# Kernel optimization log

Hardware: AMD Instinct MI355X
Metric: run time of the kernel (lower is better)

Reference implementation:

```python
import jax, jax.numpy as jnp
import numpy as np

R, B, F, H, C = 32, 2048, 512, 1024, 100  # n_rules, batch, n_fea, 2*n_fea, n_cls


def setup_inputs() -> dict:
    key = jax.random.key(0)
    ks = jax.random.split(key, 10)
    sc = lambda k, shape, fan: (jax.random.normal(k, shape, jnp.float32) / np.float32(np.sqrt(fan)))
    return {
        "data": jax.random.normal(ks[0], (B, F), jnp.float32),
        "proto": jax.random.normal(ks[1], (R, F), jnp.float32),
        "var": jax.random.uniform(ks[2], (R, F), jnp.float32, 0.5, 1.5),
        "fs_w1": sc(ks[3], (F, H), F), "fs_b1": jnp.zeros((H,), jnp.float32),
        "fs_w2": sc(ks[4], (H, F), H), "fs_b2": jnp.zeros((F,), jnp.float32),
        "fs_w3": sc(ks[5], (F, 1), F), "fs_b3": jnp.zeros((1,), jnp.float32),
        "cq_w1": sc(ks[6], (R, F, H), F), "cq_b1": jnp.zeros((R, H), jnp.float32),
        "cq_w2": sc(ks[7], (R, H, F), H), "cq_b2": jnp.zeros((R, F), jnp.float32),
        "cq_w3": sc(ks[8], (R, F, C), F), "cq_b3": jnp.zeros((R, C), jnp.float32),
        "is_train": 1,
    }


def reference(data, proto, var, fs_w1, fs_b1, fs_w2, fs_b2, fs_w3, fs_b3,
              cq_w1, cq_b1, cq_w2, cq_b2, cq_w3, cq_b3, is_train):
    # Gaussian fuzzy membership per rule: [R, B, F]
    fuzzy = jnp.exp(-(data[None, :, :] - proto[:, None, :]) ** 2
                    / (2.0 * var[:, None, :] ** 2))
    # shared fire-strength MLP applied per rule
    h = jax.nn.relu(jnp.einsum('rbf,fh->rbh', fuzzy, fs_w1) + fs_b1)
    h = jax.nn.relu(jnp.einsum('rbh,hf->rbf', h, fs_w2) + fs_b2)
    fs_logits = (jnp.einsum('rbf,fo->rbo', h, fs_w3) + fs_b3)[..., 0]  # [R, B]
    fire = jax.nn.softmax(fs_logits.T, axis=1)  # [B, R], softmax over rules
    # per-rule consequent MLPs on raw data (grouped GEMMs)
    g = jax.nn.relu(jnp.einsum('bf,rfh->rbh', data, cq_w1) + cq_b1[:, None, :])
    g = jax.nn.relu(jnp.einsum('rbh,rhf->rbf', g, cq_w2) + cq_b2[:, None, :])
    logits = jnp.einsum('rbf,rfc->rbc', g, cq_w3) + cq_b3[:, None, :]  # [R, B, C]
    # softmax-weighted expert sum, then class softmax
    out = jnp.einsum('br,rbc->bc', fire, logits)  # [B, C]
    return jax.nn.softmax(out, axis=1)
```

## Files before the change

kernel.cpp:

```cpp
#include <hip/hip_runtime.h>

typedef __attribute__((ext_vector_type(8))) short short8;
typedef __attribute__((ext_vector_type(4))) float f32x4;

__device__ __forceinline__ unsigned short f2bf(float f) {
    union { float f; unsigned u; } v; v.f = f;
    unsigned r = v.u + 0x7FFFu + ((v.u >> 16) & 1u);
    return (unsigned short)(r >> 16);
}
__device__ __forceinline__ float bf2f(unsigned short u) {
    union { unsigned u; float f; } v; v.u = ((unsigned)u) << 16;
    return v.f;
}

__global__ __launch_bounds__(256)
void cvt_bf16_kernel(const float* __restrict__ X, unsigned short* __restrict__ Y, int n4) {
    int i = blockIdx.x * 256 + threadIdx.x;
    if (i >= n4) return;
    float4 v = ((const float4*)X)[i];
    ushort4 o; o.x = f2bf(v.x); o.y = f2bf(v.y); o.z = f2bf(v.z); o.w = f2bf(v.w);
    ((ushort4*)Y)[i] = o;
}

__global__ __launch_bounds__(256)
void transpose_kernel(const float* __restrict__ X, unsigned short* __restrict__ Y,
                      int K, int N, int Np) {
    __shared__ float tile[32][33];
    int g = blockIdx.z;
    const float* Xg = X + (long)g * K * N;
    unsigned short* Yg = Y + (long)g * Np * K;
    int k0 = blockIdx.x * 32, n0 = blockIdx.y * 32;
    int tx = threadIdx.x & 31, ty = threadIdx.x >> 5;
#pragma unroll
    for (int i = 0; i < 4; ++i) {
        int kk = ty + i * 8;
        int n = n0 + tx;
        tile[kk][tx] = (n < N) ? Xg[(long)(k0 + kk) * N + n] : 0.0f;
    }
    __syncthreads();
#pragma unroll
    for (int i = 0; i < 4; ++i) {
        int nn = ty + i * 8;
        Yg[(long)(n0 + nn) * K + k0 + tx] = f2bf(tile[tx][nn]);
    }
}

__global__ __launch_bounds__(128)
void fuzzy_kernel(const float* __restrict__ data, const float* __restrict__ proto,
                  const float* __restrict__ var, unsigned short* __restrict__ fuzzy,
                  int r0) {
    int rb = blockIdx.x;
    int r = r0 + (rb >> 11), b = rb & 2047;
    int f = threadIdx.x * 4;
    float4 d = *(const float4*)(data + (long)b * 512 + f);
    float4 p = *(const float4*)(proto + (long)r * 512 + f);
    float4 w = *(const float4*)(var + (long)r * 512 + f);
    ushort4 o;
    float x;
    x = d.x - p.x; o.x = f2bf(__expf(-(x * x) / (2.f * w.x * w.x)));
    x = d.y - p.y; o.y = f2bf(__expf(-(x * x) / (2.f * w.y * w.y)));
    x = d.z - p.z; o.z = f2bf(__expf(-(x * x) / (2.f * w.z * w.z)));
    x = d.w - p.w; o.w = f2bf(__expf(-(x * x) / (2.f * w.w * w.w)));
    *(ushort4*)(fuzzy + (long)rb * 512 + f) = o;
}

template<int EPI, bool RELU>
__global__ __launch_bounds__(256, 2)
void gemm_kernel(const unsigned short* __restrict__ A,
                 const unsigned short* __restrict__ Bt,
                 const float* __restrict__ bias,
                 void* __restrict__ Cptr,
                 const float* __restrict__ w3,
                 float* __restrict__ fslog,
                 int nM, int nN, int K,
                 long sAg, long sBg, long sCg, int sBiasG, int biasN) {
    unsigned tot = gridDim.x;
    unsigned bid = blockIdx.x;
    unsigned sw = (tot & 7u) == 0 ? (bid & 7u) * (tot >> 3) + (bid >> 3) : bid;
    unsigned pg = (unsigned)nM * (unsigned)nN;
    unsigned g = sw / pg;
    unsigned rem = sw - g * pg;
    unsigned mt_ = rem / (unsigned)nN;
    unsigned nt_ = rem - mt_ * (unsigned)nN;
    const int N = nN * 128;
    A += (long)g * sAg;
    Bt += (long)g * sBg;
    bias += (long)g * sBiasG;
    const int m0 = (int)mt_ * 128;
    const int n0 = (int)nt_ * 128;

    __shared__ __align__(16) unsigned short ldsA[128 * 32];
    __shared__ __align__(16) unsigned short ldsB[128 * 32];

    const int tid = threadIdx.x;
    const int lane = tid & 63;
    const int w = tid >> 6;
    const int wm = w >> 1, wn = w & 1;
    const int r16 = lane & 15, kg = lane >> 4;

    f32x4 acc[4][4];
#pragma unroll
    for (int i = 0; i < 4; ++i)
#pragma unroll
        for (int j = 0; j < 4; ++j) {
            f32x4 z = {0.f, 0.f, 0.f, 0.f};
            acc[i][j] = z;
        }

    for (int k0 = 0; k0 < K; k0 += 32) {
#pragma unroll
        for (int j = 0; j < 2; ++j) {
            int t = j * 256 + tid;
            int row = t >> 2, kc = (t & 3) * 8;
            const unsigned short* ga = A + (long)(m0 + row) * K + k0 + kc;
            __builtin_amdgcn_global_load_lds(
                (const __attribute__((address_space(1))) void*)ga,
                (__attribute__((address_space(3))) void*)(ldsA + (j * 256 + w * 64) * 8),
                16, 0, 0);
            const unsigned short* gb = Bt + (long)(n0 + row) * K + k0 + kc;
            __builtin_amdgcn_global_load_lds(
                (const __attribute__((address_space(1))) void*)gb,
                (__attribute__((address_space(3))) void*)(ldsB + (j * 256 + w * 64) * 8),
                16, 0, 0);
        }
        __syncthreads();
        short8 aF[4], bF[4];
#pragma unroll
        for (int mt = 0; mt < 4; ++mt)
            aF[mt] = *(const short8*)(ldsA + (wm * 64 + mt * 16 + r16) * 32 + kg * 8);
#pragma unroll
        for (int nt = 0; nt < 4; ++nt)
            bF[nt] = *(const short8*)(ldsB + (wn * 64 + nt * 16 + r16) * 32 + kg * 8);
#pragma unroll
        for (int mt = 0; mt < 4; ++mt)
#pragma unroll
            for (int nt = 0; nt < 4; ++nt)
                acc[mt][nt] = __builtin_amdgcn_mfma_f32_16x16x32_bf16(
                    aF[mt], bF[nt], acc[mt][nt], 0, 0, 0);
        __syncthreads();
    }

    if constexpr (EPI == 1) {
        float w3v[4], bv[4];
#pragma unroll
        for (int nt = 0; nt < 4; ++nt) {
            int col = n0 + wn * 64 + nt * 16 + r16;
            w3v[nt] = w3[col];
            bv[nt] = bias[col];
        }
#pragma unroll
        for (int mt = 0; mt < 4; ++mt) {
#pragma unroll
            for (int j = 0; j < 4; ++j) {
                float p = 0.f;
#pragma unroll
                for (int nt = 0; nt < 4; ++nt) {
                    float v = acc[mt][nt][j] + bv[nt];
                    if (RELU) v = fmaxf(v, 0.f);
                    p += v * w3v[nt];
                }
                p += __shfl_xor(p, 1, 64);
                p += __shfl_xor(p, 2, 64);
                p += __shfl_xor(p, 4, 64);
                p += __shfl_xor(p, 8, 64);
                if (r16 == 0) {
                    int row = m0 + wm * 64 + mt * 16 + kg * 4 + j;
                    atomicAdd(&fslog[row], p);
                }
            }
        }
    } else {
#pragma unroll
        for (int nt = 0; nt < 4; ++nt) {
            int col = n0 + wn * 64 + nt * 16 + r16;
            float bv = (col < biasN) ? bias[col] : 0.f;
#pragma unroll
            for (int mt = 0; mt < 4; ++mt) {
#pragma unroll
                for (int j = 0; j < 4; ++j) {
                    int row = m0 + wm * 64 + mt * 16 + kg * 4 + j;
                    float v = acc[mt][nt][j] + bv;
                    if (RELU) v = fmaxf(v, 0.f);
                    if constexpr (EPI == 0)
                        ((unsigned short*)Cptr)[(long)g * sCg + (long)row * N + col] = f2bf(v);
                    else
                        ((float*)Cptr)[(long)g * sCg + (long)row * N + col] = v;
                }
            }
        }
    }
}

__global__ __launch_bounds__(256)
void fire_kernel(const float* __restrict__ fslog, float* __restrict__ fire) {
    int b = blockIdx.x * 256 + threadIdx.x;
    float v[32];
    float mx = -1e30f;
#pragma unroll
    for (int r = 0; r < 32; ++r) { v[r] = fslog[r * 2048 + b]; mx = fmaxf(mx, v[r]); }
    float s = 0.f;
#pragma unroll
    for (int r = 0; r < 32; ++r) { v[r] = __expf(v[r] - mx); s += v[r]; }
    float inv = 1.f / s;
#pragma unroll
    for (int r = 0; r < 32; ++r) fire[b * 32 + r] = v[r] * inv;
}

__global__ __launch_bounds__(128)
void accum_kernel(const float* __restrict__ logits, const float* __restrict__ fire,
                  float* __restrict__ mix, int r0, int NR, int first) {
    int b = blockIdx.x, c = threadIdx.x;
    float acc = first ? 0.f : mix[b * 128 + c];
    for (int r = 0; r < NR; ++r)
        acc += fire[b * 32 + r0 + r] * logits[((long)r * 2048 + b) * 128 + c];
    mix[b * 128 + c] = acc;
}

__global__ __launch_bounds__(128)
void softmax_out_kernel(const float* __restrict__ mix, float* __restrict__ out) {
    int b = blockIdx.x, c = threadIdx.x;
    __shared__ float redm[2], reds[2];
    float val = (c < 100) ? mix[b * 128 + c] : -1e30f;
    float m = val;
#pragma unroll
    for (int off = 32; off; off >>= 1) m = fmaxf(m, __shfl_xor(m, off, 64));
    int lane = c & 63, wv = c >> 6;
    if (lane == 0) redm[wv] = m;
    __syncthreads();
    m = fmaxf(redm[0], redm[1]);
    float e = (c < 100) ? __expf(val - m) : 0.f;
    float s = e;
#pragma unroll
    for (int off = 32; off; off >>= 1) s += __shfl_xor(s, off, 64);
    if (lane == 0) reds[wv] = s;
    __syncthreads();
    s = reds[0] + reds[1];
    if (c < 100) out[b * 100 + c] = e / s;
}

extern "C" void kernel_launch(void* const* d_in, const int* in_sizes, int n_in,
                              void* d_out, int out_size, void* d_ws, size_t ws_size,
                              hipStream_t stream) {
    const float* data  = (const float*)d_in[0];
    const float* proto = (const float*)d_in[1];
    const float* var   = (const float*)d_in[2];
    const float* fs_w1 = (const float*)d_in[3];
    const float* fs_b1 = (const float*)d_in[4];
    const float* fs_w2 = (const float*)d_in[5];
    const float* fs_b2 = (const float*)d_in[6];
    const float* fs_w3 = (const float*)d_in[7];
    const float* cq_w1 = (const float*)d_in[9];
    const float* cq_b1 = (const float*)d_in[10];
    const float* cq_w2 = (const float*)d_in[11];
    const float* cq_b2 = (const float*)d_in[12];
    const float* cq_w3 = (const float*)d_in[13];
    const float* cq_b3 = (const float*)d_in[14];
    float* out = (float*)d_out;

    const size_t PERSIST = 2097152 + 1048576 + 1048576 + 262144 + 262144 + 1048576;
    const size_t PER_RULE_P2 = 1048576 + 1048576 + 131072 + 2097152;
    auto need = [&](int p1r, int p2r) -> size_t {
        size_t logitsC = (size_t)p2r * 2048 * 128 * 4;
        size_t R0 = (size_t)p1r * 2048 * 512 * 2;
        size_t r0p2 = (size_t)p2r * PER_RULE_P2;
        if (r0p2 > R0) R0 = r0p2;
        size_t R1 = (size_t)p1r * 2048 * 1024 * 2;
        size_t g1b = (size_t)p2r * 2048 * 1024 * 2;
        if (g1b > R1) R1 = g1b;
        return PERSIST + logitsC + R0 + R1;
    };
    int p1r = 32, p2r = 16;
    while (need(p1r, p2r) > ws_size && p1r > 2) { p1r >>= 1; p2r >>= 1; }

    char* ws = (char*)d_ws;
    size_t off = 0;
    auto take = [&](size_t bytes) { char* p = ws + off; off += bytes; return p; };
    unsigned short* data_bf = (unsigned short*)take(2097152);
    unsigned short* w1t     = (unsigned short*)take(1048576);
    unsigned short* w2t     = (unsigned short*)take(1048576);
    float*          fslog   = (float*)take(262144);
    float*          fire    = (float*)take(262144);
    float*          mix     = (float*)take(1048576);
    float*          logitsC = (float*)take((size_t)p2r * 2048 * 128 * 4);
    size_t R0sz = (size_t)p1r * 2048 * 512 * 2;
    { size_t t = (size_t)p2r * PER_RULE_P2; if (t > R0sz) R0sz = t; }
    char* R0 = take(R0sz);
    size_t R1sz = (size_t)p1r * 2048 * 1024 * 2;
    char* R1 = take(R1sz);

    unsigned short* cF   = (unsigned short*)R0;
    unsigned short* cW1t = (unsigned short*)R0;
    unsigned short* cW2t = (unsigned short*)(R0 + (size_t)p2r * 1048576);
    unsigned short* cW3t = (unsigned short*)(R0 + (size_t)p2r * 2097152);
    unsigned short* g2   = (unsigned short*)(R0 + (size_t)p2r * 2097152 + (size_t)p2r * 131072);
    unsigned short* h1   = (unsigned short*)R1;
    unsigned short* g1   = (unsigned short*)R1;

    cvt_bf16_kernel<<<1024, 256, 0, stream>>>(data, data_bf, 262144);
    transpose_kernel<<<dim3(16, 32, 1), 256, 0, stream>>>(fs_w1, w1t, 512, 1024, 1024);
    transpose_kernel<<<dim3(32, 16, 1), 256, 0, stream>>>(fs_w2, w2t, 1024, 512, 512);
    hipMemsetAsync(fslog, 0, 262144, stream);

    for (int ch = 0; ch < 32 / p1r; ++ch) {
        const int r0 = ch * p1r;
        fuzzy_kernel<<<p1r * 2048, 128, 0, stream>>>(data, proto, var, cF, r0);
        gemm_kernel<0, true><<<p1r * 16 * 8, 256, 0, stream>>>(
            cF, w1t, fs_b1, h1, nullptr, nullptr,
            p1r * 16, 8, 512, 0, 0, 0, 0, 1024);
        gemm_kernel<1, true><<<p1r * 16 * 4, 256, 0, stream>>>(
            h1, w2t, fs_b2, nullptr, fs_w3, fslog + (long)r0 * 2048,
            p1r * 16, 4, 1024, 0, 0, 0, 0, 512);
    }
    fire_kernel<<<8, 256, 0, stream>>>(fslog, fire);

    for (int ch = 0; ch < 32 / p2r; ++ch) {
        const int r0 = ch * p2r;
        transpose_kernel<<<dim3(16, 32, p2r), 256, 0, stream>>>(
            cq_w1 + (long)r0 * 512 * 1024, cW1t, 512, 1024, 1024);
        transpose_kernel<<<dim3(32, 16, p2r), 256, 0, stream>>>(
            cq_w2 + (long)r0 * 1024 * 512, cW2t, 1024, 512, 512);
        transpose_kernel<<<dim3(16, 4, p2r), 256, 0, stream>>>(
            cq_w3 + (long)r0 * 512 * 100, cW3t, 512, 100, 128);
        gemm_kernel<0, true><<<16 * 8 * p2r, 256, 0, stream>>>(
            data_bf, cW1t, cq_b1 + (long)r0 * 1024, g1, nullptr, nullptr,
            16, 8, 512, 0, (long)1024 * 512, (long)2048 * 1024, 1024, 1024);
        gemm_kernel<0, true><<<16 * 4 * p2r, 256, 0, stream>>>(
            g1, cW2t, cq_b2 + (long)r0 * 512, g2, nullptr, nullptr,
            16, 4, 1024, (long)2048 * 1024, (long)512 * 1024, (long)2048 * 512, 512, 512);
        gemm_kernel<2, false><<<16 * 1 * p2r, 256, 0, stream>>>(
            g2, cW3t, cq_b3 + (long)r0 * 100, logitsC, nullptr, nullptr,
            16, 1, 512, (long)2048 * 512, (long)128 * 512, (long)2048 * 128, 100, 100);
        accum_kernel<<<2048, 128, 0, stream>>>(logitsC, fire, mix, r0, p2r, ch == 0);
    }
    softmax_out_kernel<<<2048, 128, 0, stream>>>(mix, out);
}
```

Measured before the change: 549.8 us.

## Swizzle LDS tiles, stage GEMM output via LDS, fuse fire-weighted accumulation into GEMM

GEMM tiles in LDS now use an XOR swizzle on the k-chunk index, meant to cut bank conflicts on fragment reads. The bf16 epilogue is staged through a padded LDS tile so global stores become coalesced 16-byte writes. The separate accumulation kernel is removed: the final consequent GEMM atomically adds fire-weighted logits into the mix buffer, so the logitsC buffer is no longer written. The fire-strength path now processes all 32 rules in a single launch instead of chunks. These changes cost extra LDS per block and add many float atomics, and the atomic accumulation order is no longer fixed.

```diff
diff --git a/kernel.cpp b/kernel.cpp
--- a/kernel.cpp
+++ b/kernel.cpp
@@ -7,10 +7,6 @@
     union { float f; unsigned u; } v; v.f = f;
     unsigned r = v.u + 0x7FFFu + ((v.u >> 16) & 1u);
     return (unsigned short)(r >> 16);
-}
-__device__ __forceinline__ float bf2f(unsigned short u) {
-    union { unsigned u; float f; } v; v.u = ((unsigned)u) << 16;
-    return v.f;
 }
 
 __global__ __launch_bounds__(256)
@@ -47,10 +43,9 @@
 
 __global__ __launch_bounds__(128)
 void fuzzy_kernel(const float* __restrict__ data, const float* __restrict__ proto,
-                  const float* __restrict__ var, unsigned short* __restrict__ fuzzy,
-                  int r0) {
+                  const float* __restrict__ var, unsigned short* __restrict__ fuzzy) {
     int rb = blockIdx.x;
-    int r = r0 + (rb >> 11), b = rb & 2047;
+    int r = rb >> 11, b = rb & 2047;
     int f = threadIdx.x * 4;
     float4 d = *(const float4*)(data + (long)b * 512 + f);
     float4 p = *(const float4*)(proto + (long)r * 512 + f);
@@ -66,28 +61,24 @@
 
 template<int EPI, bool RELU>
 __global__ __launch_bounds__(256, 2)
-void gemm_kernel(const unsigned short* __restrict__ A,
-                 const unsigned short* __restrict__ Bt,
-                 const float* __restrict__ bias,
-                 void* __restrict__ Cptr,
-                 const float* __restrict__ w3,
-                 float* __restrict__ fslog,
-                 int nM, int nN, int K,
-                 long sAg, long sBg, long sCg, int sBiasG, int biasN) {
-    unsigned tot = gridDim.x;
-    unsigned bid = blockIdx.x;
-    unsigned sw = (tot & 7u) == 0 ? (bid & 7u) * (tot >> 3) + (bid >> 3) : bid;
+void gemm128_kernel(const unsigned short* __restrict__ A,
+                    const unsigned short* __restrict__ Bt,
+                    const float* __restrict__ bias,
+                    void* __restrict__ Cptr,
+                    const float* __restrict__ w3,
+                    float* __restrict__ fsl_or_mix,
+                    const float* __restrict__ fire,
+                    int nM, int nN, int K,
+                    long sAg, long sBg, long sCg, int sBiasG, int biasN, int r0) {
+    unsigned tot = gridDim.x, bid = blockIdx.x;
+    unsigned sw = (bid & 7u) * (tot >> 3) + (bid >> 3);
     unsigned pg = (unsigned)nM * (unsigned)nN;
     unsigned g = sw / pg;
     unsigned rem = sw - g * pg;
-    unsigned mt_ = rem / (unsigned)nN;
-    unsigned nt_ = rem - mt_ * (unsigned)nN;
+    const int m0 = (int)(rem / (unsigned)nN) * 128;
+    const int n0 = (int)(rem % (unsigned)nN) * 128;
     const int N = nN * 128;
-    A += (long)g * sAg;
-    Bt += (long)g * sBg;
-    bias += (long)g * sBiasG;
-    const int m0 = (int)mt_ * 128;
-    const int n0 = (int)nt_ * 128;
+    A += (long)g * sAg; Bt += (long)g * sBg; bias += (long)g * sBiasG;
 
     __shared__ __align__(16) unsigned short ldsA[128 * 32];
     __shared__ __align__(16) unsigned short ldsB[128 * 32];
@@ -111,26 +102,31 @@
 #pragma unroll
         for (int j = 0; j < 2; ++j) {
             int t = j * 256 + tid;
-            int row = t >> 2, kc = (t & 3) * 8;
+            int row = t >> 2, sl = t & 3;
+            int kc = (sl ^ ((row >> 1) & 3)) << 3;
             const unsigned short* ga = A + (long)(m0 + row) * K + k0 + kc;
             __builtin_amdgcn_global_load_lds(
                 (const __attribute__((address_space(1))) void*)ga,
-                (__attribute__((address_space(3))) void*)(ldsA + (j * 256 + w * 64) * 8),
+                (__attribute__((address_space(3))) void*)(ldsA + (j * 256 + tid) * 8),
                 16, 0, 0);
             const unsigned short* gb = Bt + (long)(n0 + row) * K + k0 + kc;
             __builtin_amdgcn_global_load_lds(
                 (const __attribute__((address_space(1))) void*)gb,
-                (__attribute__((address_space(3))) void*)(ldsB + (j * 256 + w * 64) * 8),
+                (__attribute__((address_space(3))) void*)(ldsB + (j * 256 + tid) * 8),
                 16, 0, 0);
         }
         __syncthreads();
         short8 aF[4], bF[4];
 #pragma unroll
-        for (int mt = 0; mt < 4; ++mt)
-            aF[mt] = *(const short8*)(ldsA + (wm * 64 + mt * 16 + r16) * 32 + kg * 8);
-#pragma unroll
-        for (int nt = 0; nt < 4; ++nt)
-            bF[nt] = *(const short8*)(ldsB + (wn * 64 + nt * 16 + r16) * 32 + kg * 8);
+        for (int mt = 0; mt < 4; ++mt) {
+            int R = wm * 64 + mt * 16 + r16;
+            aF[mt] = *(const short8*)(ldsA + R * 32 + ((kg ^ ((R >> 1) & 3)) << 3));
+        }
+#pragma unroll
+        for (int nt = 0; nt < 4; ++nt) {
+            int R = wn * 64 + nt * 16 + r16;
+            bF[nt] = *(const short8*)(ldsB + R * 32 + ((kg ^ ((R >> 1) & 3)) << 3));
+        }
 #pragma unroll
         for (int mt = 0; mt < 4; ++mt)
 #pragma unroll
@@ -165,28 +161,60 @@
                 p += __shfl_xor(p, 8, 64);
                 if (r16 == 0) {
                     int row = m0 + wm * 64 + mt * 16 + kg * 4 + j;
-                    atomicAdd(&fslog[row], p);
+                    atomicAdd(&fsl_or_mix[row], p);
                 }
             }
         }
-    } else {
+    } else if constexpr (EPI == 3) {
+        float bv[4];
 #pragma unroll
         for (int nt = 0; nt < 4; ++nt) {
             int col = n0 + wn * 64 + nt * 16 + r16;
-            float bv = (col < biasN) ? bias[col] : 0.f;
-#pragma unroll
-            for (int mt = 0; mt < 4; ++mt) {
-#pragma unroll
-                for (int j = 0; j < 4; ++j) {
-                    int row = m0 + wm * 64 + mt * 16 + kg * 4 + j;
-                    float v = acc[mt][nt][j] + bv;
-                    if (RELU) v = fmaxf(v, 0.f);
-                    if constexpr (EPI == 0)
-                        ((unsigned short*)Cptr)[(long)g * sCg + (long)row * N + col] = f2bf(v);
-                    else
-                        ((float*)Cptr)[(long)g * sCg + (long)row * N + col] = v;
+            bv[nt] = (col < biasN) ? bias[col] : 0.f;
+        }
+#pragma unroll
+        for (int mt = 0; mt < 4; ++mt) {
+#pragma unroll
+            for (int j = 0; j < 4; ++j) {
+                int row = m0 + wm * 64 + mt * 16 + kg * 4 + j;
+                float f = fire[row * 32 + r0 + (int)g];
+#pragma unroll
+                for (int nt = 0; nt < 4; ++nt) {
+                    int col = n0 + wn * 64 + nt * 16 + r16;
+                    atomicAdd(&fsl_or_mix[row * 128 + col], f * (acc[mt][nt][j] + bv[nt]));
                 }
             }
+        }
+    } else {
+        __shared__ __align__(16) unsigned short ldsC[128 * 136];
+        float bv[4];
+#pragma unroll
+        for (int nt = 0; nt < 4; ++nt) {
+            int col = n0 + wn * 64 + nt * 16 + r16;
+            bv[nt] = (col < biasN) ? bias[col] : 0.f;
+        }
+#pragma unroll
+        for (int mt = 0; mt < 4; ++mt) {
+            int rl = wm * 64 + mt * 16 + kg * 4;
+#pragma unroll
+            for (int nt = 0; nt < 4; ++nt) {
+                int cc = wn * 64 + nt * 16 + r16;
+#pragma unroll
+                for (int j = 0; j < 4; ++j) {
+                    float v = acc[mt][nt][j] + bv[nt];
+                    if (RELU) v = fmaxf(v, 0.f);
+                    ldsC[(rl + j) * 136 + cc] = f2bf(v);
+                }
+            }
+        }
+        __syncthreads();
+        unsigned short* Cg = (unsigned short*)Cptr + (long)g * sCg;
+#pragma unroll
+        for (int rnd = 0; rnd < 8; ++rnd) {
+            int idx = rnd * 256 + tid;
+            int row = idx >> 4, c8 = idx & 15;
+            short8 vv = *(const short8*)(ldsC + row * 136 + c8 * 8);
+            *(short8*)(Cg + (long)(m0 + row) * N + n0 + c8 * 8) = vv;
         }
     }
 }
@@ -204,16 +232,6 @@
     float inv = 1.f / s;
 #pragma unroll
     for (int r = 0; r < 32; ++r) fire[b * 32 + r] = v[r] * inv;
-}
-
-__global__ __launch_bounds__(128)
-void accum_kernel(const float* __restrict__ logits, const float* __restrict__ fire,
-                  float* __restrict__ mix, int r0, int NR, int first) {
-    int b = blockIdx.x, c = threadIdx.x;
-    float acc = first ? 0.f : mix[b * 128 + c];
-    for (int r = 0; r < NR; ++r)
-        acc += fire[b * 32 + r0 + r] * logits[((long)r * 2048 + b) * 128 + c];
-    mix[b * 128 + c] = acc;
 }
 
 __global__ __launch_bounds__(128)
@@ -258,19 +276,14 @@
     float* out = (float*)d_out;
 
     const size_t PERSIST = 2097152 + 1048576 + 1048576 + 262144 + 262144 + 1048576;
-    const size_t PER_RULE_P2 = 1048576 + 1048576 + 131072 + 2097152;
-    auto need = [&](int p1r, int p2r) -> size_t {
-        size_t logitsC = (size_t)p2r * 2048 * 128 * 4;
-        size_t R0 = (size_t)p1r * 2048 * 512 * 2;
-        size_t r0p2 = (size_t)p2r * PER_RULE_P2;
-        if (r0p2 > R0) R0 = r0p2;
-        size_t R1 = (size_t)p1r * 2048 * 1024 * 2;
-        size_t g1b = (size_t)p2r * 2048 * 1024 * 2;
-        if (g1b > R1) R1 = g1b;
-        return PERSIST + logitsC + R0 + R1;
+    const size_t H1SZ = (size_t)65536 * 1024 * 2;
+    const size_t FUZZSZ = (size_t)65536 * 512 * 2;
+    auto need = [&](int p) -> size_t {
+        size_t fz = FUZZSZ > (size_t)p * 2097152 ? FUZZSZ : (size_t)p * 2097152;
+        return PERSIST + H1SZ + fz + (size_t)p * (1048576 + 1048576 + 131072);
     };
-    int p1r = 32, p2r = 16;
-    while (need(p1r, p2r) > ws_size && p1r > 2) { p1r >>= 1; p2r >>= 1; }
+    int p2r = 16;
+    while (need(p2r) > ws_size && p2r > 2) p2r >>= 1;
 
     char* ws = (char*)d_ws;
     size_t off = 0;
@@ -281,36 +294,28 @@
     float*          fslog   = (float*)take(262144);
     float*          fire    = (float*)take(262144);
     float*          mix     = (float*)take(1048576);
-    float*          logitsC = (float*)take((size_t)p2r * 2048 * 128 * 4);
-    size_t R0sz = (size_t)p1r * 2048 * 512 * 2;
-    { size_t t = (size_t)p2r * PER_RULE_P2; if (t > R0sz) R0sz = t; }
-    char* R0 = take(R0sz);
-    size_t R1sz = (size_t)p1r * 2048 * 1024 * 2;
-    char* R1 = take(R1sz);
-
-    unsigned short* cF   = (unsigned short*)R0;
-    unsigned short* cW1t = (unsigned short*)R0;
-    unsigned short* cW2t = (unsigned short*)(R0 + (size_t)p2r * 1048576);
-    unsigned short* cW3t = (unsigned short*)(R0 + (size_t)p2r * 2097152);
-    unsigned short* g2   = (unsigned short*)(R0 + (size_t)p2r * 2097152 + (size_t)p2r * 131072);
-    unsigned short* h1   = (unsigned short*)R1;
-    unsigned short* g1   = (unsigned short*)R1;
+    unsigned short* h1      = (unsigned short*)take(H1SZ);
+    size_t fzsz = FUZZSZ > (size_t)p2r * 2097152 ? FUZZSZ : (size_t)p2r * 2097152;
+    unsigned short* fuzzy   = (unsigned short*)take(fzsz);
+    unsigned short* cW1t    = (unsigned short*)take((size_t)p2r * 1048576);
+    unsigned short* cW2t    = (unsigned short*)take((size_t)p2r * 1048576);
+    unsigned short* cW3t    = (unsigned short*)take((size_t)p2r * 131072);
+    unsigned short* g1 = h1;
+    unsigned short* g2 = fuzzy;
 
     cvt_bf16_kernel<<<1024, 256, 0, stream>>>(data, data_bf, 262144);
     transpose_kernel<<<dim3(16, 32, 1), 256, 0, stream>>>(fs_w1, w1t, 512, 1024, 1024);
     transpose_kernel<<<dim3(32, 16, 1), 256, 0, stream>>>(fs_w2, w2t, 1024, 512, 512);
     hipMemsetAsync(fslog, 0, 262144, stream);
-
-    for (int ch = 0; ch < 32 / p1r; ++ch) {
-        const int r0 = ch * p1r;
-        fuzzy_kernel<<<p1r * 2048, 128, 0, stream>>>(data, proto, var, cF, r0);
-        gemm_kernel<0, true><<<p1r * 16 * 8, 256, 0, stream>>>(
-            cF, w1t, fs_b1, h1, nullptr, nullptr,
-            p1r * 16, 8, 512, 0, 0, 0, 0, 1024);
-        gemm_kernel<1, true><<<p1r * 16 * 4, 256, 0, stream>>>(
-            h1, w2t, fs_b2, nullptr, fs_w3, fslog + (long)r0 * 2048,
-            p1r * 16, 4, 1024, 0, 0, 0, 0, 512);
-    }
+    hipMemsetAsync(mix, 0, 1048576, stream);
+
+    fuzzy_kernel<<<65536, 128, 0, stream>>>(data, proto, var, fuzzy);
+    gemm128_kernel<0, true><<<512 * 8, 256, 0, stream>>>(
+        fuzzy, w1t, fs_b1, h1, nullptr, nullptr, nullptr,
+        512, 8, 512, 0, 0, 0, 0, 1024, 0);
+    gemm128_kernel<1, true><<<512 * 4, 256, 0, stream>>>(
+        h1, w2t, fs_b2, nullptr, fs_w3, fslog, nullptr,
+        512, 4, 1024, 0, 0, 0, 0, 512, 0);
     fire_kernel<<<8, 256, 0, stream>>>(fslog, fire);
 
     for (int ch = 0; ch < 32 / p2r; ++ch) {
@@ -321,16 +326,15 @@
             cq_w2 + (long)r0 * 1024 * 512, cW2t, 1024, 512, 512);
         transpose_kernel<<<dim3(16, 4, p2r), 256, 0, stream>>>(
             cq_w3 + (long)r0 * 512 * 100, cW3t, 512, 100, 128);
-        gemm_kernel<0, true><<<16 * 8 * p2r, 256, 0, stream>>>(
-            data_bf, cW1t, cq_b1 + (long)r0 * 1024, g1, nullptr, nullptr,
-            16, 8, 512, 0, (long)1024 * 512, (long)2048 * 1024, 1024, 1024);
-        gemm_kernel<0, true><<<16 * 4 * p2r, 256, 0, stream>>>(
-            g1, cW2t, cq_b2 + (long)r0 * 512, g2, nullptr, nullptr,
-            16, 4, 1024, (long)2048 * 1024, (long)512 * 1024, (long)2048 * 512, 512, 512);
-        gemm_kernel<2, false><<<16 * 1 * p2r, 256, 0, stream>>>(
-            g2, cW3t, cq_b3 + (long)r0 * 100, logitsC, nullptr, nullptr,
-            16, 1, 512, (long)2048 * 512, (long)128 * 512, (long)2048 * 128, 100, 100);
-        accum_kernel<<<2048, 128, 0, stream>>>(logitsC, fire, mix, r0, p2r, ch == 0);
+        gemm128_kernel<0, true><<<16 * 8 * p2r, 256, 0, stream>>>(
+            data_bf, cW1t, cq_b1 + (long)r0 * 1024, g1, nullptr, nullptr, nullptr,
+            16, 8, 512, 0, (long)1024 * 512, (long)2048 * 1024, 1024, 1024, 0);
+        gemm128_kernel<0, true><<<16 * 4 * p2r, 256, 0, stream>>>(
+            g1, cW2t, cq_b2 + (long)r0 * 512, g2, nullptr, nullptr, nullptr,
+            16, 4, 1024, (long)2048 * 1024, (long)512 * 1024, (long)2048 * 512, 512, 512, 0);
+        gemm128_kernel<3, false><<<16 * 1 * p2r, 256, 0, stream>>>(
+            g2, cW3t, cq_b3 + (long)r0 * 100, nullptr, nullptr, mix, fire,
+            16, 1, 512, (long)2048 * 512, (long)128 * 512, 0, 100, 100, r0);
     }
     softmax_out_kernel<<<2048, 128, 0, stream>>>(mix, out);
 }
```

Result: slower. 571.6 us (+4.0%).
